# Optimization experiments

Measured on AMD Instinct MI355X. Metric: run time of the kernel, lower is better.

The kernel has to match this reference:

```python
import jax, jax.numpy as jnp
import numpy as np

N = 8192
X_DIM = 256
Y_DIM = 256


def setup_inputs() -> dict:
    key = jax.random.key(0)
    kx, ky, kw = jax.random.split(key, 3)
    x_samples = jax.random.normal(kx, (N, X_DIM), dtype=jnp.float32)
    y_samples = jax.random.normal(ky, (N, Y_DIM), dtype=jnp.float32)
    # kaiming-uniform-ish init for the bilinear weight [x_dim, y_dim]
    bound = float(np.sqrt(6.0 / X_DIM))
    w = jax.random.uniform(kw, (X_DIM, Y_DIM), dtype=jnp.float32,
                           minval=-bound, maxval=bound)
    return {"x_samples": x_samples, "y_samples": y_samples, "w": w}


def reference(x_samples, y_samples, w):
    # Pairwise bilinear scores S[i, b] = x[i] @ W @ y[b]
    # (equivalent to the original's tiled einsum, without O(N^2*dim) tiles)
    n = y_samples.shape[0]
    xw = x_samples @ w                      # [N, y_dim]
    S = xw @ y_samples.T                    # [N, N], S[i, b]
    # T0[i] = S[i, i]; T1.logsumexp(dim=1)[b] = logsumexp_i S[i, b]
    t0_mean = jnp.mean(jnp.diagonal(S))
    lse_mean = jnp.mean(jax.nn.logsumexp(S, axis=0))
    lower_bound = t0_mean - (lse_mean - jnp.log(jnp.float32(n)))
    return lower_bound
```

## Files before the change

### kernel.cpp

```cpp
#include <hip/hip_runtime.h>

typedef __attribute__((ext_vector_type(8))) short bf16x8;
typedef __attribute__((ext_vector_type(4))) float f32x4;
typedef __attribute__((ext_vector_type(8))) int   i32x8;
typedef __attribute__((ext_vector_type(4))) int   i32x4;

union OpU { i32x8 v; i32x4 h[2]; };

__device__ __forceinline__ unsigned short f2bf(float f) {
    unsigned int u = __float_as_uint(f);
    u += 0x7fffu + ((u >> 16) & 1u);
    return (unsigned short)(u >> 16);
}

#define LSE_SHIFT   90.0f
#define LOG2E       1.44269504f
#define SHIFT_L2E   129.842553f

__global__ void cast_wy_kernel(const float* __restrict__ y, const float* __restrict__ w,
                               unsigned char* __restrict__ YQ, unsigned short* __restrict__ WT,
                               float* __restrict__ scal)
{
    int idx = blockIdx.x * 256 + threadIdx.x;
    const float4 yv = ((const float4*)y)[idx];
    int pk = __builtin_amdgcn_cvt_pk_fp8_f32(yv.x, yv.y, 0, 0);
    pk     = __builtin_amdgcn_cvt_pk_fp8_f32(yv.z, yv.w, pk, 1);
    ((int*)YQ)[idx] = pk;
    if (idx < 16384) {
        const float4 wv = ((const float4*)w)[idx];
        int k = idx >> 6;
        int n0 = (idx & 63) * 4;
        WT[(size_t)(n0 + 0) * 256 + k] = f2bf(wv.x);
        WT[(size_t)(n0 + 1) * 256 + k] = f2bf(wv.y);
        WT[(size_t)(n0 + 2) * 256 + k] = f2bf(wv.z);
        WT[(size_t)(n0 + 3) * 256 + k] = f2bf(wv.w);
    }
    if (idx == 0) {
        scal[0] = 0.f; scal[1] = 0.f;
        ((unsigned int*)scal)[2] = 0u;
    }
}

__global__ __launch_bounds__(256, 4)
void gemm0_kernel(const float* __restrict__ X, const unsigned short* __restrict__ WT,
                  unsigned char* __restrict__ XWQ)
{
    __shared__ __align__(16) unsigned short As[64 * 64];
    __shared__ __align__(16) unsigned short Bs[64 * 64];

    const int tid  = threadIdx.x;
    const int lane = tid & 63;
    const int w    = tid >> 6;
    const int wm   = w >> 1, wn = w & 1;
    const int frow = lane & 15, quad = lane >> 4;
    const int rowBase = blockIdx.y * 64;
    const int colBase = blockIdx.x * 64;

    int aOff[2][2], bOff[2][2];
#pragma unroll
    for (int mi = 0; mi < 2; ++mi)
#pragma unroll
        for (int kk = 0; kk < 2; ++kk) {
            int ka = kk * 4 + quad;
            int ra = wm * 32 + mi * 16 + frow;
            aOff[mi][kk] = ra * 64 + ((ka ^ (ra & 7)) << 3);
            int rb = wn * 32 + mi * 16 + frow;
            bOff[mi][kk] = rb * 64 + ((ka ^ (rb & 7)) << 3);
        }

    f32x4 acc[2][2];
#pragma unroll
    for (int i = 0; i < 2; ++i)
#pragma unroll
        for (int j = 0; j < 2; ++j)
            acc[i][j] = f32x4{0.f, 0.f, 0.f, 0.f};

#pragma unroll
    for (int kt = 0; kt < 4; ++kt) {
        const int k0 = kt * 64;
#pragma unroll
        for (int it = 0; it < 2; ++it) {
            int p  = it * 256 + tid;
            int r  = p >> 3;
            int s  = p & 7;
            int kc = s ^ (r & 7);
            const unsigned short* gb = WT + (size_t)(colBase + r) * 256 + k0 + (kc << 3);
            __builtin_amdgcn_global_load_lds(
                (const __attribute__((address_space(1))) void*)gb,
                (__attribute__((address_space(3))) void*)&Bs[p << 3], 16, 0, 0);
        }
#pragma unroll
        for (int it = 0; it < 4; ++it) {
            int fidx = it * 256 + tid;
            int r  = fidx >> 4;
            int c4 = fidx & 15;
            float4 v = *(const float4*)&X[(size_t)(rowBase + r) * 256 + k0 + c4 * 4];
            ushort4 u;
            u.x = f2bf(v.x); u.y = f2bf(v.y); u.z = f2bf(v.z); u.w = f2bf(v.w);
            int slot = (c4 >> 1) ^ (r & 7);
            *(ushort4*)&As[r * 64 + (slot << 3) + (c4 & 1) * 4] = u;
        }
        __syncthreads();
#pragma unroll
        for (int kk = 0; kk < 2; ++kk) {
            bf16x8 a[2], b[2];
#pragma unroll
            for (int mi = 0; mi < 2; ++mi) a[mi] = *(const bf16x8*)&As[aOff[mi][kk]];
#pragma unroll
            for (int ni = 0; ni < 2; ++ni) b[ni] = *(const bf16x8*)&Bs[bOff[ni][kk]];
#pragma unroll
            for (int mi = 0; mi < 2; ++mi)
#pragma unroll
                for (int ni = 0; ni < 2; ++ni)
                    acc[mi][ni] = __builtin_amdgcn_mfma_f32_16x16x32_bf16(
                        a[mi], b[ni], acc[mi][ni], 0, 0, 0);
        }
        __syncthreads();
    }

#pragma unroll
    for (int mi = 0; mi < 2; ++mi)
#pragma unroll
        for (int ni = 0; ni < 2; ++ni)
#pragma unroll
            for (int r2 = 0; r2 < 4; ++r2) {
                int row = rowBase + wm * 32 + mi * 16 + quad * 4 + r2;
                int col = colBase + wn * 32 + ni * 16 + frow;
                float v = acc[mi][ni][r2];
                int q = __builtin_amdgcn_cvt_pk_fp8_f32(v, v, 0, 0);
                XWQ[(size_t)row * 256 + col] = (unsigned char)(q & 0xff);
            }
}

__global__ __launch_bounds__(256, 3)
void gemm1_kernel(const unsigned char* __restrict__ A,
                  const unsigned char* __restrict__ B,
                  float* __restrict__ P, float* __restrict__ scal)
{
    __shared__ __align__(16) unsigned char As[128 * 128];
    __shared__ __align__(16) unsigned char Bs[128 * 128];
    __shared__ float lsebuf[256];

    const int tid  = threadIdx.x;
    const int lane = tid & 63;
    const int w    = tid >> 6;
    const int wm   = w >> 1, wn = w & 1;
    const int frow = lane & 15, quad = lane >> 4;
    const int rowBase = blockIdx.y * 128;
    const int colBase = blockIdx.x * 128;

    const unsigned char* gaP[4];
    const unsigned char* gbP[4];
    unsigned int ldsP[4];
#pragma unroll
    for (int it = 0; it < 4; ++it) {
        int p  = it * 256 + tid;
        int r  = p >> 3;
        int s  = p & 7;
        int kc = s ^ (r & 7);
        gaP[it] = A + (size_t)(rowBase + r) * 256 + (kc << 4);
        gbP[it] = B + (size_t)(colBase + r) * 256 + (kc << 4);
        ldsP[it] = p << 4;
    }
    const int c0 = quad * 2;
    int aAdr[4][2], bAdr[4][2];
#pragma unroll
    for (int mi = 0; mi < 4; ++mi) {
        int ra = wm * 64 + mi * 16 + frow;
        aAdr[mi][0] = ra * 128 + ((c0 ^ (ra & 7)) << 4);
        aAdr[mi][1] = ra * 128 + (((c0 + 1) ^ (ra & 7)) << 4);
        int rb = wn * 64 + mi * 16 + frow;
        bAdr[mi][0] = rb * 128 + ((c0 ^ (rb & 7)) << 4);
        bAdr[mi][1] = rb * 128 + (((c0 + 1) ^ (rb & 7)) << 4);
    }

    f32x4 acc[4][4];
#pragma unroll
    for (int i = 0; i < 4; ++i)
#pragma unroll
        for (int j = 0; j < 4; ++j)
            acc[i][j] = f32x4{0.f, 0.f, 0.f, 0.f};

#pragma unroll
    for (int kt = 0; kt < 2; ++kt) {
#pragma unroll
        for (int it = 0; it < 4; ++it) {
            __builtin_amdgcn_global_load_lds(
                (const __attribute__((address_space(1))) void*)gaP[it],
                (__attribute__((address_space(3))) void*)&As[ldsP[it]], 16, 0, 0);
            __builtin_amdgcn_global_load_lds(
                (const __attribute__((address_space(1))) void*)gbP[it],
                (__attribute__((address_space(3))) void*)&Bs[ldsP[it]], 16, 0, 0);
            gaP[it] += 128;
            gbP[it] += 128;
        }
        __syncthreads();

        i32x8 a[4], b[4];
#pragma unroll
        for (int mi = 0; mi < 4; ++mi) {
            OpU u;
            u.h[0] = *(const i32x4*)&As[aAdr[mi][0]];
            u.h[1] = *(const i32x4*)&As[aAdr[mi][1]];
            a[mi] = u.v;
        }
#pragma unroll
        for (int ni = 0; ni < 4; ++ni) {
            OpU u;
            u.h[0] = *(const i32x4*)&Bs[bAdr[ni][0]];
            u.h[1] = *(const i32x4*)&Bs[bAdr[ni][1]];
            b[ni] = u.v;
        }
#pragma unroll
        for (int mi = 0; mi < 4; ++mi)
#pragma unroll
            for (int ni = 0; ni < 4; ++ni)
                acc[mi][ni] = __builtin_amdgcn_mfma_scale_f32_16x16x128_f8f6f4(
                    a[mi], b[ni], acc[mi][ni],
                    0, 0,
                    0, 0x7f7f7f7f,
                    0, 0x7f7f7f7f);
        __syncthreads();
    }

#pragma unroll
    for (int ni = 0; ni < 4; ++ni) {
        float ssum = 0.f;
#pragma unroll
        for (int mi = 0; mi < 4; ++mi)
#pragma unroll
            for (int r2 = 0; r2 < 4; ++r2)
                ssum += __builtin_amdgcn_exp2f(
                    __fmaf_rn(acc[mi][ni][r2], LOG2E, -SHIFT_L2E));
        ssum += __shfl_xor(ssum, 16);
        ssum += __shfl_xor(ssum, 32);
        if (quad == 0)
            lsebuf[wm * 128 + wn * 64 + ni * 16 + frow] = ssum;
    }
    if (blockIdx.x == blockIdx.y && wm == wn) {
        float v = 0.f;
#pragma unroll
        for (int mi = 0; mi < 4; ++mi)
#pragma unroll
            for (int r2 = 0; r2 < 4; ++r2)
                if (quad * 4 + r2 == frow) v += acc[mi][mi][r2];
#pragma unroll
        for (int o = 1; o < 64; o <<= 1) v += __shfl_xor(v, o);
        if (lane == 0) atomicAdd(&scal[0], v);
    }
    __syncthreads();
    if (tid < 128) {
        float s = lsebuf[tid] + lsebuf[128 + tid];
        P[(size_t)blockIdx.y * 8192 + colBase + tid] = LSE_SHIFT + __logf(s);
    }
}

__global__ void combine_kernel(const float* __restrict__ P, float* __restrict__ scal,
                               float* __restrict__ out)
{
    __shared__ float red[256];
    const int tid = threadIdx.x;
    const int col = blockIdx.x * 256 + tid;
    float m = -1e30f, s = 0.f;
#pragma unroll 8
    for (int j = 0; j < 64; ++j) {
        float v = P[(size_t)j * 8192 + col];
        float nm = fmaxf(m, v);
        s = s * __expf(m - nm) + __expf(v - nm);
        m = nm;
    }
    red[tid] = m + logf(s);
    __syncthreads();
#pragma unroll
    for (int o = 128; o > 0; o >>= 1) {
        if (tid < o) red[tid] += red[tid + o];
        __syncthreads();
    }
    if (tid == 0) {
        atomicAdd(&scal[1], red[0]);
        __threadfence();
        unsigned int old = __hip_atomic_fetch_add((unsigned int*)&scal[2], 1u,
                                                  __ATOMIC_ACQ_REL, __HIP_MEMORY_SCOPE_AGENT);
        if (old == 31u) {
            float t0 = __hip_atomic_load(&scal[0], __ATOMIC_RELAXED, __HIP_MEMORY_SCOPE_AGENT);
            float ls = __hip_atomic_load(&scal[1], __ATOMIC_RELAXED, __HIP_MEMORY_SCOPE_AGENT);
            const float invN = 1.f / 8192.f;
            out[0] = t0 * invN - (ls * invN - logf(8192.f));
        }
    }
}

extern "C" void kernel_launch(void* const* d_in, const int* in_sizes, int n_in,
                              void* d_out, int out_size, void* d_ws, size_t ws_size,
                              hipStream_t stream)
{
    const float* x = (const float*)d_in[0];
    const float* y = (const float*)d_in[1];
    const float* w = (const float*)d_in[2];
    float* out = (float*)d_out;

    char* ws = (char*)d_ws;
    unsigned char*  YQ  = (unsigned char*)(ws);
    unsigned char*  XWQ = (unsigned char*)(ws + 0x200000);
    unsigned short* WT  = (unsigned short*)(ws + 0x400000);
    float*          P   = (float*)        (ws + 0x420000);
    float*          scal= (float*)        (ws + 0x620000);

    cast_wy_kernel<<<2048, 256, 0, stream>>>(y, w, YQ, WT, scal);
    gemm0_kernel<<<dim3(4, 128), 256, 0, stream>>>(x, WT, XWQ);
    gemm1_kernel<<<dim3(64, 64), 256, 0, stream>>>(XWQ, YQ, P, scal);
    combine_kernel<<<32, 256, 0, stream>>>(P, scal, out);
}
```

Baseline: 107.4 us.

## Stage full-K A tile in LDS once and load B fragments directly from global

The A tile for all of K is loaded into shared memory in a single pass using a 16-way XOR swizzle, replacing the two-stage loop with its per-iteration barriers. The B operand skips shared memory: each lane reads its MFMA fragment directly from global memory. This cuts barriers and LDS traffic for B. In exchange, B reads are duplicated across waves and rely on the cache, and the direct global loads may add latency before the MFMAs.

```diff
diff --git a/kernel.cpp b/kernel.cpp
--- a/kernel.cpp
+++ b/kernel.cpp
@@ -137,8 +137,7 @@
                   const unsigned char* __restrict__ B,
                   float* __restrict__ P, float* __restrict__ scal)
 {
-    __shared__ __align__(16) unsigned char As[128 * 128];
-    __shared__ __align__(16) unsigned char Bs[128 * 128];
+    __shared__ __align__(16) unsigned char As[128 * 256];
     __shared__ float lsebuf[256];
 
     const int tid  = threadIdx.x;
@@ -149,29 +148,23 @@
     const int rowBase = blockIdx.y * 128;
     const int colBase = blockIdx.x * 128;
 
-    const unsigned char* gaP[4];
-    const unsigned char* gbP[4];
-    unsigned int ldsP[4];
-#pragma unroll
-    for (int it = 0; it < 4; ++it) {
+#pragma unroll
+    for (int it = 0; it < 8; ++it) {
         int p  = it * 256 + tid;
-        int r  = p >> 3;
-        int s  = p & 7;
-        int kc = s ^ (r & 7);
-        gaP[it] = A + (size_t)(rowBase + r) * 256 + (kc << 4);
-        gbP[it] = B + (size_t)(colBase + r) * 256 + (kc << 4);
-        ldsP[it] = p << 4;
-    }
-    const int c0 = quad * 2;
-    int aAdr[4][2], bAdr[4][2];
-#pragma unroll
-    for (int mi = 0; mi < 4; ++mi) {
-        int ra = wm * 64 + mi * 16 + frow;
-        aAdr[mi][0] = ra * 128 + ((c0 ^ (ra & 7)) << 4);
-        aAdr[mi][1] = ra * 128 + (((c0 + 1) ^ (ra & 7)) << 4);
-        int rb = wn * 64 + mi * 16 + frow;
-        bAdr[mi][0] = rb * 128 + ((c0 ^ (rb & 7)) << 4);
-        bAdr[mi][1] = rb * 128 + (((c0 + 1) ^ (rb & 7)) << 4);
+        int r  = p >> 4;
+        int s  = p & 15;
+        int kc = s ^ (r & 15);
+        const unsigned char* ga = A + (size_t)(rowBase + r) * 256 + (kc << 4);
+        __builtin_amdgcn_global_load_lds(
+            (const __attribute__((address_space(1))) void*)ga,
+            (__attribute__((address_space(3))) void*)&As[p << 4], 16, 0, 0);
+    }
+
+    const unsigned char* bP[4];
+#pragma unroll
+    for (int ni = 0; ni < 4; ++ni) {
+        int rb = colBase + wn * 64 + ni * 16 + frow;
+        bP[ni] = B + (size_t)rb * 256 + quad * 32;
     }
 
     f32x4 acc[4][4];
@@ -181,35 +174,32 @@
         for (int j = 0; j < 4; ++j)
             acc[i][j] = f32x4{0.f, 0.f, 0.f, 0.f};
 
+    __syncthreads();
+
 #pragma unroll
     for (int kt = 0; kt < 2; ++kt) {
-#pragma unroll
-        for (int it = 0; it < 4; ++it) {
-            __builtin_amdgcn_global_load_lds(
-                (const __attribute__((address_space(1))) void*)gaP[it],
-                (__attribute__((address_space(3))) void*)&As[ldsP[it]], 16, 0, 0);
-            __builtin_amdgcn_global_load_lds(
-                (const __attribute__((address_space(1))) void*)gbP[it],
-                (__attribute__((address_space(3))) void*)&Bs[ldsP[it]], 16, 0, 0);
-            gaP[it] += 128;
-            gbP[it] += 128;
-        }
-        __syncthreads();
-
-        i32x8 a[4], b[4];
-#pragma unroll
-        for (int mi = 0; mi < 4; ++mi) {
-            OpU u;
-            u.h[0] = *(const i32x4*)&As[aAdr[mi][0]];
-            u.h[1] = *(const i32x4*)&As[aAdr[mi][1]];
-            a[mi] = u.v;
-        }
+        i32x8 b[4];
 #pragma unroll
         for (int ni = 0; ni < 4; ++ni) {
             OpU u;
-            u.h[0] = *(const i32x4*)&Bs[bAdr[ni][0]];
-            u.h[1] = *(const i32x4*)&Bs[bAdr[ni][1]];
+            if (kt == 0) {
+                u.h[0] = *(const i32x4*)(bP[ni]);
+                u.h[1] = *(const i32x4*)(bP[ni] + 16);
+            } else {
+                u.h[0] = *(const i32x4*)(bP[ni] + 128);
+                u.h[1] = *(const i32x4*)(bP[ni] + 144);
+            }
             b[ni] = u.v;
+        }
+        i32x8 a[4];
+#pragma unroll
+        for (int mi = 0; mi < 4; ++mi) {
+            int ra = wm * 64 + mi * 16 + frow;
+            int c0 = kt * 8 + quad * 2;
+            OpU u;
+            u.h[0] = *(const i32x4*)&As[ra * 256 + ((c0 ^ frow) << 4)];
+            u.h[1] = *(const i32x4*)&As[ra * 256 + (((c0 + 1) ^ frow) << 4)];
+            a[mi] = u.v;
         }
 #pragma unroll
         for (int mi = 0; mi < 4; ++mi)
@@ -220,7 +210,6 @@
                     0, 0,
                     0, 0x7f7f7f7f,
                     0, 0x7f7f7f7f);
-        __syncthreads();
     }
 
 #pragma unroll
```

Result: slower. 120.8 us (+12.5%).
